# Optimization experiments

Measured on AMD Instinct MI355X. Metric: run time of the kernel, lower is better.

Reference implementation:

```python
import jax, jax.numpy as jnp
import numpy as np

N_NODES = 100000

def _gcn_norm(edge_index, num_nodes):
    # add self-loops, compute symmetric normalization coeffs per edge
    loops = jnp.arange(num_nodes, dtype=edge_index.dtype)
    src = jnp.concatenate([edge_index[0], loops])
    dst = jnp.concatenate([edge_index[1], loops])
    deg = jax.ops.segment_sum(jnp.ones_like(dst, dtype=jnp.float32), dst,
                              num_segments=num_nodes)
    dinv = jnp.where(deg > 0, jax.lax.rsqrt(deg), 0.0)
    norm = dinv[src] * dinv[dst]  # [E + N]
    return src, dst, norm

def _gcn_conv(x, W, b, src, dst, norm, num_nodes):
    h = x @ W                              # [N, out] transform first (PyG order)
    msg = h[src] * norm[:, None]           # gather + scale
    out = jax.ops.segment_sum(msg, dst, num_segments=num_nodes)  # scatter-add
    return out + b

def setup_inputs() -> dict:
    key = jax.random.key(0)
    k1, k2, k3, k4 = jax.random.split(key, 4)
    F_in, H, C = 128, 64, 40
    x = jax.random.normal(k1, (N_NODES, F_in), dtype=jnp.float32)
    edge_index = jax.random.randint(k2, (2, 1600000), 0, N_NODES, dtype=jnp.int64)
    W1 = jax.random.normal(k3, (F_in, H), dtype=jnp.float32) / np.sqrt(F_in)
    b1 = jnp.zeros((H,), dtype=jnp.float32)
    W2 = jax.random.normal(k4, (H, C), dtype=jnp.float32) / np.sqrt(H)
    b2 = jnp.zeros((C,), dtype=jnp.float32)
    return {"x": x, "edge_index": edge_index, "W1": W1, "b1": b1, "W2": W2, "b2": b2}

def reference(x, edge_index, W1, b1, W2, b2):
    num_nodes = x.shape[0]
    src, dst, norm = _gcn_norm(edge_index, num_nodes)
    h = _gcn_conv(x, W1, b1, src, dst, norm, num_nodes)
    h = jax.nn.relu(h)
    # dropout is identity in eval mode (training=False)
    h = _gcn_conv(h, W2, b2, src, dst, norm, num_nodes)
    return jax.nn.log_softmax(h, axis=1)
```

## Files before the change

### kernel.cpp

```cpp
#include <hip/hip_runtime.h>
#include <math.h>

#define NPB 256
#define BSH 8
#define MAXNB 400
#define BIN_CHUNK 8192
#define HIST_CHUNK 16384

typedef __attribute__((ext_vector_type(8))) short bf16x8;
typedef __attribute__((ext_vector_type(4))) float f32x4;
typedef __attribute__((ext_vector_type(2))) float f32x2;

__device__ __forceinline__ unsigned short f2bf(float f){
  unsigned int u = __float_as_uint(f);
  unsigned int r = (u + 0x7FFFu + ((u >> 16) & 1u)) >> 16;
  return (unsigned short)r;
}

__device__ __forceinline__ bf16x8 cvt8(float4 a, float4 b){
  union { unsigned u[4]; bf16x8 v; } r;
  asm("v_cvt_pk_bf16_f32 %0, %1, %2" : "=v"(r.u[0]) : "v"(a.x), "v"(a.y));
  asm("v_cvt_pk_bf16_f32 %0, %1, %2" : "=v"(r.u[1]) : "v"(a.z), "v"(a.w));
  asm("v_cvt_pk_bf16_f32 %0, %1, %2" : "=v"(r.u[2]) : "v"(b.x), "v"(b.y));
  asm("v_cvt_pk_bf16_f32 %0, %1, %2" : "=v"(r.u[3]) : "v"(b.z), "v"(b.w));
  return r.v;
}

__global__ void k_prep(const float* __restrict__ W1, const float* __restrict__ W2,
                       unsigned short* __restrict__ w1t, unsigned short* __restrict__ w2t,
                       int* __restrict__ bcnt, int NB){
  int t = threadIdx.x;
  if(blockIdx.x == 0){
    for(int i = t; i < 8192; i += 256){
      int k = i >> 6, f = i & 63;
      w1t[f*128 + k] = f2bf(W1[i]);
    }
  } else {
    for(int i = t; i < 3072; i += 256){
      int c = i >> 6, k = i & 63;
      w2t[c*64 + k] = (c < 40) ? f2bf(W2[k*40 + c]) : (unsigned short)0;
    }
    for(int i = t; i < NB; i += 256) bcnt[i] = 0;
  }
}


__global__ __launch_bounds__(256) void k_bhist(const int* __restrict__ dst, int E,
                                               int* __restrict__ bcnt, int NB){
  __shared__ int l[MAXNB];
  int t = threadIdx.x;
  int base = blockIdx.x*HIST_CHUNK;
  int end = base + HIST_CHUNK; if(end > E) end = E;
  for(int b = t; b < NB; b += 256) l[b] = 0;
  __syncthreads();
  for(int i = base + t; i < end; i += 256) atomicAdd(&l[dst[i] >> BSH], 1);
  __syncthreads();
  for(int b = t; b < NB; b += 256){ int c = l[b]; if(c) atomicAdd(&bcnt[b], c); }
}

__global__ void k_bscan(const int* __restrict__ bcnt, int* __restrict__ bofs,
                        int* __restrict__ bcur, int NB, int E){
  __shared__ int sh[1024];
  int t = threadIdx.x;
  int c0 = (2*t   < NB) ? bcnt[2*t]   : 0;
  int c1 = (2*t+1 < NB) ? bcnt[2*t+1] : 0;
  sh[t] = c0 + c1; __syncthreads();
  for(int off = 1; off < 1024; off <<= 1){
    int v = (t >= off) ? sh[t - off] : 0;
    __syncthreads();
    sh[t] += v;
    __syncthreads();
  }
  int pairEx = sh[t] - (c0 + c1);
  if(2*t   < NB){ bofs[2*t]   = pairEx;      bcur[2*t]   = pairEx; }
  if(2*t+1 < NB){ bofs[2*t+1] = pairEx + c0; bcur[2*t+1] = pairEx + c0; }
  if(t == 0) bofs[NB] = E;
}

__global__ __launch_bounds__(256) void k_binpass(const int* __restrict__ src,
                          const int* __restrict__ dst, int E,
                          int* __restrict__ bcur, unsigned int* __restrict__ binned, int NB){
  __shared__ int lcnt[MAXNB];
  __shared__ int lpos[MAXNB];
  int t = threadIdx.x;
  int base = blockIdx.x * BIN_CHUNK;
  int end = base + BIN_CHUNK; if(end > E) end = E;
  for(int b = t; b < NB; b += 256) lcnt[b] = 0;
  __syncthreads();
  for(int i = base + t; i < end; i += 256)
    atomicAdd(&lcnt[dst[i] >> BSH], 1);
  __syncthreads();
  for(int b = t; b < NB; b += 256){
    int c = lcnt[b];
    lpos[b] = c ? atomicAdd(&bcur[b], c) : 0;
  }
  __syncthreads();
  for(int i = base + t; i < end; i += 256){
    int d = dst[i];
    int b = d >> BSH;
    unsigned int rec = (unsigned int)src[i] | ((unsigned int)(d & (NPB-1)) << 17);
    int p = atomicAdd(&lpos[b], 1);
    binned[p] = rec;
  }
}

__global__ __launch_bounds__(256) void k_bscatter(const unsigned int* __restrict__ binned,
     const int* __restrict__ bofs, int* __restrict__ csr, int* __restrict__ row_ofs,
     float* __restrict__ dinv, int N, int E, int NB){
  __shared__ int lcnt[NPB];
  __shared__ int lofs[NPB];
  __shared__ int lcur[NPB];
  __shared__ int wsum[4];
  int b = blockIdx.x, t = threadIdx.x;
  int beg = bofs[b], end = bofs[b+1];
  lcnt[t] = 0;
  __syncthreads();
  for(int i = beg + t; i < end; i += 256) atomicAdd(&lcnt[binned[i] >> 17], 1);
  __syncthreads();
  int c = lcnt[t];
  int lane = t & 63, wid = t >> 6;
  int v = c;
  #pragma unroll
  for(int off = 1; off < 64; off <<= 1){
    int nv = __shfl_up(v, off, 64);
    if(lane >= off) v += nv;
  }
  if(lane == 63) wsum[wid] = v;
  __syncthreads();
  int wpre = 0;
  #pragma unroll
  for(int k2 = 0; k2 < 4; k2++) if(k2 < wid) wpre += wsum[k2];
  int ex = wpre + v - c;
  lofs[t] = beg + ex; lcur[t] = 0;
  int node = (b << BSH) + t;
  if(node < N){
    row_ofs[node] = beg + ex;
    dinv[node] = rsqrtf((float)(c + 1));
  }
  __syncthreads();
  for(int i = beg + t; i < end; i += 256){
    unsigned int rec = binned[i];
    int dl = rec >> 17;
    int pos = lofs[dl] + atomicAdd(&lcur[dl], 1);
    csr[pos] = (int)(rec & 0x1FFFFu);
  }
  if(b == NB-1 && t == 0) row_ofs[N] = E;
}

__global__ __launch_bounds__(256) void k_gemm1(const float* __restrict__ x,
                        const unsigned short* __restrict__ w1t,
                        const float* __restrict__ dinv, unsigned int* __restrict__ g1, int n){
  __shared__ unsigned short xs[128*136];
  __shared__ unsigned short wt[64*136];
  int tid = threadIdx.x;
  int nodeBase = blockIdx.x*128;
  for(int i = tid; i < 1024; i += 256){
    int f = i >> 4, seg = i & 15;
    *(uint4*)&wt[f*136 + seg*8] = *(const uint4*)&w1t[f*128 + seg*8];
  }
  {
    const float4* x4 = (const float4*)x;
    for(int i = tid; i < 2048; i += 256){
      int node = i >> 4, seg = i & 15;
      float4 va = make_float4(0.f,0.f,0.f,0.f), vb = va;
      if(nodeBase + node < n){
        va = x4[(size_t)(nodeBase + node)*32 + seg*2];
        vb = x4[(size_t)(nodeBase + node)*32 + seg*2 + 1];
      }
      *(bf16x8*)&xs[node*136 + seg*8] = cvt8(va, vb);
    }
  }
  __syncthreads();

  int w = tid >> 6, lane = tid & 63;
  int ml = lane & 15, q = lane >> 4;
  int n0 = nodeBase + w*32 + ml;
  int n1 = n0 + 16;
  bool vn0 = n0 < n, vn1 = n1 < n;

  f32x4 a00 = {0.f,0.f,0.f,0.f}, a01 = {0.f,0.f,0.f,0.f},
        a02 = {0.f,0.f,0.f,0.f}, a03 = {0.f,0.f,0.f,0.f};
  f32x4 a10 = {0.f,0.f,0.f,0.f}, a11 = {0.f,0.f,0.f,0.f},
        a12 = {0.f,0.f,0.f,0.f}, a13 = {0.f,0.f,0.f,0.f};
  const unsigned short* brow = &xs[(w*32 + ml)*136 + q*8];
  const unsigned short* arow = &wt[ml*136 + q*8];
  #pragma unroll
  for(int s = 0; s < 4; s++){
    bf16x8 bb0 = *(const bf16x8*)(brow +        s*32);
    bf16x8 bb1 = *(const bf16x8*)(brow + 2176 + s*32);
    bf16x8 a0 = *(const bf16x8*)(arow +    0 + s*32);
    bf16x8 a1 = *(const bf16x8*)(arow + 2176 + s*32);
    bf16x8 a2 = *(const bf16x8*)(arow + 4352 + s*32);
    bf16x8 a3 = *(const bf16x8*)(arow + 6528 + s*32);
    a00 = __builtin_amdgcn_mfma_f32_16x16x32_bf16(a0, bb0, a00, 0, 0, 0);
    a01 = __builtin_amdgcn_mfma_f32_16x16x32_bf16(a1, bb0, a01, 0, 0, 0);
    a02 = __builtin_amdgcn_mfma_f32_16x16x32_bf16(a2, bb0, a02, 0, 0, 0);
    a03 = __builtin_amdgcn_mfma_f32_16x16x32_bf16(a3, bb0, a03, 0, 0, 0);
    a10 = __builtin_amdgcn_mfma_f32_16x16x32_bf16(a0, bb1, a10, 0, 0, 0);
    a11 = __builtin_amdgcn_mfma_f32_16x16x32_bf16(a1, bb1, a11, 0, 0, 0);
    a12 = __builtin_amdgcn_mfma_f32_16x16x32_bf16(a2, bb1, a12, 0, 0, 0);
    a13 = __builtin_amdgcn_mfma_f32_16x16x32_bf16(a3, bb1, a13, 0, 0, 0);
  }
  if(vn0){
    float dv = dinv[n0];
    unsigned base16 = ((unsigned)n0 << 4) + q;
    int p;
    p = __builtin_amdgcn_cvt_pk_fp8_f32(a00[0]*dv, a00[1]*dv, 0, false);
    p = __builtin_amdgcn_cvt_pk_fp8_f32(a00[2]*dv, a00[3]*dv, p, true);
    g1[base16 +  0] = (unsigned)p;
    p = __builtin_amdgcn_cvt_pk_fp8_f32(a01[0]*dv, a01[1]*dv, 0, false);
    p = __builtin_amdgcn_cvt_pk_fp8_f32(a01[2]*dv, a01[3]*dv, p, true);
    g1[base16 +  4] = (unsigned)p;
    p = __builtin_amdgcn_cvt_pk_fp8_f32(a02[0]*dv, a02[1]*dv, 0, false);
    p = __builtin_amdgcn_cvt_pk_fp8_f32(a02[2]*dv, a02[3]*dv, p, true);
    g1[base16 +  8] = (unsigned)p;
    p = __builtin_amdgcn_cvt_pk_fp8_f32(a03[0]*dv, a03[1]*dv, 0, false);
    p = __builtin_amdgcn_cvt_pk_fp8_f32(a03[2]*dv, a03[3]*dv, p, true);
    g1[base16 + 12] = (unsigned)p;
  }
  if(vn1){
    float dv = dinv[n1];
    unsigned base16 = ((unsigned)n1 << 4) + q;
    int p;
    p = __builtin_amdgcn_cvt_pk_fp8_f32(a10[0]*dv, a10[1]*dv, 0, false);
    p = __builtin_amdgcn_cvt_pk_fp8_f32(a10[2]*dv, a10[3]*dv, p, true);
    g1[base16 +  0] = (unsigned)p;
    p = __builtin_amdgcn_cvt_pk_fp8_f32(a11[0]*dv, a11[1]*dv, 0, false);
    p = __builtin_amdgcn_cvt_pk_fp8_f32(a11[2]*dv, a11[3]*dv, p, true);
    g1[base16 +  4] = (unsigned)p;
    p = __builtin_amdgcn_cvt_pk_fp8_f32(a12[0]*dv, a12[1]*dv, 0, false);
    p = __builtin_amdgcn_cvt_pk_fp8_f32(a12[2]*dv, a12[3]*dv, p, true);
    g1[base16 +  8] = (unsigned)p;
    p = __builtin_amdgcn_cvt_pk_fp8_f32(a13[0]*dv, a13[1]*dv, 0, false);
    p = __builtin_amdgcn_cvt_pk_fp8_f32(a13[2]*dv, a13[3]*dv, p, true);
    g1[base16 + 12] = (unsigned)p;
  }
}

__global__ __launch_bounds__(256) void k_agg1(const unsigned* __restrict__ g1,
    const int* __restrict__ row_ofs, const int* __restrict__ csr,
    const float* __restrict__ dinv, const float* __restrict__ b1,
    unsigned short* __restrict__ u, int N){
  int t = threadIdx.x;
  int lane = t & 63;
  int f = lane & 15;
  int bq = (lane & 48) << 2;
  int node = blockIdx.x*16 + (t >> 4);
  if(node >= N) return;
  int beg = row_ofs[node], end = row_ofs[node+1];
  unsigned v = g1[((unsigned)node << 4) + f];
  f32x2 s01 = __builtin_amdgcn_cvt_pk_f32_fp8(v, false);
  f32x2 s23 = __builtin_amdgcn_cvt_pk_f32_fp8(v, true);
  for(int e = beg; e < end; e += 16){
    int rem = end - e; if(rem > 16) rem = 16;
    int idxv = (f < rem) ? csr[e + f] : 0;
    int j = 0;
    for(; j + 4 <= rem; j += 4){
      int r0 = __builtin_amdgcn_ds_bpermute(bq + ((j+0) << 2), idxv);
      int r1 = __builtin_amdgcn_ds_bpermute(bq + ((j+1) << 2), idxv);
      int r2 = __builtin_amdgcn_ds_bpermute(bq + ((j+2) << 2), idxv);
      int r3 = __builtin_amdgcn_ds_bpermute(bq + ((j+3) << 2), idxv);
      unsigned v0 = g1[((unsigned)r0 << 4) + f];
      unsigned v1 = g1[((unsigned)r1 << 4) + f];
      unsigned v2 = g1[((unsigned)r2 << 4) + f];
      unsigned v3 = g1[((unsigned)r3 << 4) + f];
      s01 += __builtin_amdgcn_cvt_pk_f32_fp8(v0, false);
      s23 += __builtin_amdgcn_cvt_pk_f32_fp8(v0, true);
      s01 += __builtin_amdgcn_cvt_pk_f32_fp8(v1, false);
      s23 += __builtin_amdgcn_cvt_pk_f32_fp8(v1, true);
      s01 += __builtin_amdgcn_cvt_pk_f32_fp8(v2, false);
      s23 += __builtin_amdgcn_cvt_pk_f32_fp8(v2, true);
      s01 += __builtin_amdgcn_cvt_pk_f32_fp8(v3, false);
      s23 += __builtin_amdgcn_cvt_pk_f32_fp8(v3, true);
    }
    for(; j < rem; j++){
      int r0 = __builtin_amdgcn_ds_bpermute(bq + (j << 2), idxv);
      unsigned v0 = g1[((unsigned)r0 << 4) + f];
      s01 += __builtin_amdgcn_cvt_pk_f32_fp8(v0, false);
      s23 += __builtin_amdgcn_cvt_pk_f32_fp8(v0, true);
    }
  }
  float dv = dinv[node];
  float4 bb = ((const float4*)b1)[f];
  float h0 = fmaxf(fmaf(dv, s01.x, bb.x), 0.f);
  float h1 = fmaxf(fmaf(dv, s01.y, bb.y), 0.f);
  float h2 = fmaxf(fmaf(dv, s23.x, bb.z), 0.f);
  float h3 = fmaxf(fmaf(dv, s23.y, bb.w), 0.f);
  unsigned p0 = (unsigned)f2bf(dv*h0) | ((unsigned)f2bf(dv*h1) << 16);
  unsigned p1 = (unsigned)f2bf(dv*h2) | ((unsigned)f2bf(dv*h3) << 16);
  ((uint2*)u)[((unsigned)node << 4) + f] = make_uint2(p0, p1);
}

__global__ __launch_bounds__(256) void k_gemm2(const unsigned short* __restrict__ u,
                        const unsigned short* __restrict__ w2t,
                        unsigned char* __restrict__ g2, int n){
  __shared__ unsigned short us[64*72];
  __shared__ unsigned short ws2[48*72];
  int t = threadIdx.x;
  int nodeBase = blockIdx.x*64;
  for(int i = t; i < 512; i += 256){
    int row = i >> 3, seg = i & 7;
    uint4 v = make_uint4(0,0,0,0);
    if(nodeBase + row < n) v = *(const uint4*)&u[(size_t)(nodeBase + row)*64 + seg*8];
    *(uint4*)&us[row*72 + seg*8] = v;
  }
  for(int i = t; i < 384; i += 256){
    int row = i >> 3, seg = i & 7;
    *(uint4*)&ws2[row*72 + seg*8] = *(const uint4*)&w2t[row*64 + seg*8];
  }
  __syncthreads();
  int w = t >> 6, lane = t & 63;
  int ml = lane & 15, q = lane >> 4;
  f32x4 acc0 = {0.f,0.f,0.f,0.f}, acc1 = {0.f,0.f,0.f,0.f}, acc2 = {0.f,0.f,0.f,0.f};
  const unsigned short* brow = &us[(w*16 + ml)*72 + q*8];
  const unsigned short* a0r = &ws2[ml*72 + q*8];
  #pragma unroll
  for(int s = 0; s < 2; s++){
    bf16x8 bb = *(const bf16x8*)(brow + s*32);
    bf16x8 a0 = *(const bf16x8*)(a0r +    0 + s*32);
    bf16x8 a1 = *(const bf16x8*)(a0r + 1152 + s*32);
    bf16x8 a2 = *(const bf16x8*)(a0r + 2304 + s*32);
    acc0 = __builtin_amdgcn_mfma_f32_16x16x32_bf16(a0, bb, acc0, 0, 0, 0);
    acc1 = __builtin_amdgcn_mfma_f32_16x16x32_bf16(a1, bb, acc1, 0, 0, 0);
    acc2 = __builtin_amdgcn_mfma_f32_16x16x32_bf16(a2, bb, acc2, 0, 0, 0);
  }
  int node = nodeBase + w*16 + ml;
  if(node < n){
    unsigned* gd = (unsigned*)g2;
    unsigned rb = (unsigned)node*10u + q;
    int p;
    p = __builtin_amdgcn_cvt_pk_fp8_f32(acc0[0], acc0[1], 0, false);
    p = __builtin_amdgcn_cvt_pk_fp8_f32(acc0[2], acc0[3], p, true);
    gd[rb + 0] = (unsigned)p;
    p = __builtin_amdgcn_cvt_pk_fp8_f32(acc1[0], acc1[1], 0, false);
    p = __builtin_amdgcn_cvt_pk_fp8_f32(acc1[2], acc1[3], p, true);
    gd[rb + 4] = (unsigned)p;
    if(q < 2){
      p = __builtin_amdgcn_cvt_pk_fp8_f32(acc2[0], acc2[1], 0, false);
      p = __builtin_amdgcn_cvt_pk_fp8_f32(acc2[2], acc2[3], p, true);
      gd[rb + 8] = (unsigned)p;
    }
  }
}

__global__ __launch_bounds__(256) void k_agg2(const unsigned char* __restrict__ g2,
     const int* __restrict__ row_ofs, const int* __restrict__ csr,
     const float* __restrict__ dinv, const float* __restrict__ b2,
     float* __restrict__ out, int N){
  int t = threadIdx.x;
  int lane = t & 63;
  int f = lane & 15;
  int fc = (f < 10) ? f : 0;
  int bq = (lane & 48) << 2;
  int node = blockIdx.x*16 + (t >> 4);
  if(node >= N) return;
  int beg = row_ofs[node], end = row_ofs[node+1];
  const unsigned* gd = (const unsigned*)g2;
  unsigned v = gd[(unsigned)node*10u + fc];
  f32x2 s01 = __builtin_amdgcn_cvt_pk_f32_fp8(v, false);
  f32x2 s23 = __builtin_amdgcn_cvt_pk_f32_fp8(v, true);
  for(int e = beg; e < end; e += 16){
    int rem = end - e; if(rem > 16) rem = 16;
    int idxv = (f < rem) ? csr[e + f] : 0;
    int j = 0;
    for(; j + 4 <= rem; j += 4){
      int r0 = __builtin_amdgcn_ds_bpermute(bq + ((j+0) << 2), idxv);
      int r1 = __builtin_amdgcn_ds_bpermute(bq + ((j+1) << 2), idxv);
      int r2 = __builtin_amdgcn_ds_bpermute(bq + ((j+2) << 2), idxv);
      int r3 = __builtin_amdgcn_ds_bpermute(bq + ((j+3) << 2), idxv);
      unsigned v0 = gd[(unsigned)r0*10u + fc];
      unsigned v1 = gd[(unsigned)r1*10u + fc];
      unsigned v2 = gd[(unsigned)r2*10u + fc];
      unsigned v3 = gd[(unsigned)r3*10u + fc];
      s01 += __builtin_amdgcn_cvt_pk_f32_fp8(v0, false);
      s23 += __builtin_amdgcn_cvt_pk_f32_fp8(v0, true);
      s01 += __builtin_amdgcn_cvt_pk_f32_fp8(v1, false);
      s23 += __builtin_amdgcn_cvt_pk_f32_fp8(v1, true);
      s01 += __builtin_amdgcn_cvt_pk_f32_fp8(v2, false);
      s23 += __builtin_amdgcn_cvt_pk_f32_fp8(v2, true);
      s01 += __builtin_amdgcn_cvt_pk_f32_fp8(v3, false);
      s23 += __builtin_amdgcn_cvt_pk_f32_fp8(v3, true);
    }
    for(; j < rem; j++){
      int r0 = __builtin_amdgcn_ds_bpermute(bq + (j << 2), idxv);
      unsigned v0 = gd[(unsigned)r0*10u + fc];
      s01 += __builtin_amdgcn_cvt_pk_f32_fp8(v0, false);
      s23 += __builtin_amdgcn_cvt_pk_f32_fp8(v0, true);
    }
  }
  float dv = dinv[node];
  float4 bb = ((const float4*)b2)[fc];
  float l0 = fmaf(dv, s01.x, bb.x);
  float l1 = fmaf(dv, s01.y, bb.y);
  float l2 = fmaf(dv, s23.x, bb.z);
  float l3 = fmaf(dv, s23.y, bb.w);
  bool valid = (f < 10);
  float m = valid ? fmaxf(fmaxf(l0,l1), fmaxf(l2,l3)) : -INFINITY;
  m = fmaxf(m, __shfl_xor(m,1,64)); m = fmaxf(m, __shfl_xor(m,2,64));
  m = fmaxf(m, __shfl_xor(m,4,64)); m = fmaxf(m, __shfl_xor(m,8,64));
  float ex = valid ? (expf(l0-m)+expf(l1-m)) + (expf(l2-m)+expf(l3-m)) : 0.f;
  ex += __shfl_xor(ex,1,64); ex += __shfl_xor(ex,2,64);
  ex += __shfl_xor(ex,4,64); ex += __shfl_xor(ex,8,64);
  float ll = logf(ex);
  if(valid){
    ((float4*)out)[(unsigned)node*10u + f] = make_float4(l0-m-ll, l1-m-ll, l2-m-ll, l3-m-ll);
  }
}


extern "C" void kernel_launch(void* const* d_in, const int* in_sizes, int n_in,
                              void* d_out, int out_size, void* d_ws, size_t ws_size,
                              hipStream_t stream){
  const float* x  = (const float*)d_in[0];
  const int*   ei = (const int*)  d_in[1];
  const float* W1 = (const float*)d_in[2];
  const float* b1 = (const float*)d_in[3];
  const float* W2 = (const float*)d_in[4];
  const float* b2 = (const float*)d_in[5];
  float* out = (float*)d_out;

  int N = in_sizes[0] / 128;
  int E = in_sizes[1] / 2;
  const int* src = ei;
  const int* dst = ei + E;
  int NB = (N + NPB - 1) >> BSH;

  char* w = (char*)d_ws;
  auto alloc = [&](size_t bytes) -> char* {
    char* p = w;
    w += (bytes + 511) & ~(size_t)511;
    return p;
  };
  int*   bcnt    = (int*)  alloc((size_t)NB*4);
  int*   bofs    = (int*)  alloc((size_t)(NB+1)*4);
  int*   bcur    = (int*)  alloc((size_t)NB*4);
  int*   row_ofs = (int*)  alloc((size_t)(N+1)*4);
  float* dinv    = (float*)alloc((size_t)N*4);
  unsigned int* binned = (unsigned int*)alloc((size_t)E*4);
  int*   csr     = (int*)  alloc((size_t)E*4);
  unsigned int*   g1 = (unsigned int*)  alloc((size_t)N*64);
  unsigned short* u  = (unsigned short*)alloc((size_t)N*64*2);
  unsigned char*  g2 = (unsigned char*) alloc((size_t)N*40);
  unsigned short* w1t = (unsigned short*)alloc((size_t)64*128*2);
  unsigned short* w2t = (unsigned short*)alloc((size_t)48*64*2);

  k_prep    <<<2, 256, 0, stream>>>(W1, W2, w1t, w2t, bcnt, NB);
  k_bhist   <<<(E+HIST_CHUNK-1)/HIST_CHUNK, 256, 0, stream>>>(dst, E, bcnt, NB);
  k_bscan   <<<1, 1024, 0, stream>>>(bcnt, bofs, bcur, NB, E);
  k_binpass <<<(E+BIN_CHUNK-1)/BIN_CHUNK, 256, 0, stream>>>(src, dst, E, bcur, binned, NB);
  k_bscatter<<<NB, 256, 0, stream>>>(binned, bofs, csr, row_ofs, dinv, N, E, NB);

  k_gemm1   <<<(N+127)/128, 256, 0, stream>>>(x, w1t, dinv, g1, N);
  k_agg1    <<<(N+15)/16, 256, 0, stream>>>(g1, row_ofs, csr, dinv, b1, u, N);
  k_gemm2   <<<(N+63)/64, 256, 0, stream>>>(u, w2t, g2, N);
  k_agg2    <<<(N+15)/16, 256, 0, stream>>>(g2, row_ofs, csr, dinv, b2, out, N);
}
```

Baseline: 232.3 us.

## Replace binned CSR build with global-atomic counting sort; fuse agg1 into gemm2

The two-level bin-then-scatter CSR construction is replaced by per-node global atomic degree counting, a three-kernel scan, and a direct atomic scatter of source indices into CSR. This drops the intermediate binned buffer and its extra pass, at the cost of global atomics on random destinations. Separately, the layer-1 aggregation is fused into the layer-2 GEMM kernel, which writes aggregated rows into shared memory. That removes the round trip of the intermediate u tensor through global memory but cuts aggregation parallelism to 64 nodes per block.

```diff
diff --git a/kernel.cpp b/kernel.cpp
--- a/kernel.cpp
+++ b/kernel.cpp
@@ -1,11 +1,7 @@
 #include <hip/hip_runtime.h>
 #include <math.h>
 
-#define NPB 256
-#define BSH 8
-#define MAXNB 400
-#define BIN_CHUNK 8192
-#define HIST_CHUNK 16384
+#define HIST_CHUNK 8192
 
 typedef __attribute__((ext_vector_type(8))) short bf16x8;
 typedef __attribute__((ext_vector_type(4))) float f32x4;
@@ -28,42 +24,52 @@
 
 __global__ void k_prep(const float* __restrict__ W1, const float* __restrict__ W2,
                        unsigned short* __restrict__ w1t, unsigned short* __restrict__ w2t,
-                       int* __restrict__ bcnt, int NB){
-  int t = threadIdx.x;
-  if(blockIdx.x == 0){
+                       int* __restrict__ deg, int NPAD){
+  int t = threadIdx.x, b = blockIdx.x;
+  if(b == 0){
     for(int i = t; i < 8192; i += 256){
       int k = i >> 6, f = i & 63;
       w1t[f*128 + k] = f2bf(W1[i]);
     }
-  } else {
+  } else if(b == 1){
     for(int i = t; i < 3072; i += 256){
       int c = i >> 6, k = i & 63;
       w2t[c*64 + k] = (c < 40) ? f2bf(W2[k*40 + c]) : (unsigned short)0;
     }
-    for(int i = t; i < NB; i += 256) bcnt[i] = 0;
-  }
-}
-
-
-__global__ __launch_bounds__(256) void k_bhist(const int* __restrict__ dst, int E,
-                                               int* __restrict__ bcnt, int NB){
-  __shared__ int l[MAXNB];
-  int t = threadIdx.x;
+  } else {
+    int i = (b-2)*256 + t;
+    if(i < NPAD) deg[i] = 0;
+  }
+}
+
+
+__global__ __launch_bounds__(256) void k_hist(const int* __restrict__ dst, int E,
+                                              int* __restrict__ deg){
   int base = blockIdx.x*HIST_CHUNK;
   int end = base + HIST_CHUNK; if(end > E) end = E;
-  for(int b = t; b < NB; b += 256) l[b] = 0;
+  for(int i = base + threadIdx.x; i < end; i += 256)
+    atomicAdd(&deg[dst[i]], 1);
+}
+
+__global__ __launch_bounds__(256) void k_s1(const int* __restrict__ deg,
+                                            int* __restrict__ bsum){
+  __shared__ int ws[4];
+  int b = blockIdx.x, t = threadIdx.x;
+  int v = deg[b*256 + t];
+  v += __shfl_down(v, 32, 64); v += __shfl_down(v, 16, 64);
+  v += __shfl_down(v,  8, 64); v += __shfl_down(v,  4, 64);
+  v += __shfl_down(v,  2, 64); v += __shfl_down(v,  1, 64);
+  if((t & 63) == 0) ws[t >> 6] = v;
   __syncthreads();
-  for(int i = base + t; i < end; i += 256) atomicAdd(&l[dst[i] >> BSH], 1);
-  __syncthreads();
-  for(int b = t; b < NB; b += 256){ int c = l[b]; if(c) atomicAdd(&bcnt[b], c); }
-}
-
-__global__ void k_bscan(const int* __restrict__ bcnt, int* __restrict__ bofs,
-                        int* __restrict__ bcur, int NB, int E){
+  if(t == 0) bsum[b] = ws[0] + ws[1] + ws[2] + ws[3];
+}
+
+__global__ void k_s2(const int* __restrict__ bsum, int* __restrict__ bofs,
+                     int NBK, int E){
   __shared__ int sh[1024];
   int t = threadIdx.x;
-  int c0 = (2*t   < NB) ? bcnt[2*t]   : 0;
-  int c1 = (2*t+1 < NB) ? bcnt[2*t+1] : 0;
+  int c0 = (2*t   < NBK) ? bsum[2*t]   : 0;
+  int c1 = (2*t+1 < NBK) ? bsum[2*t+1] : 0;
   sh[t] = c0 + c1; __syncthreads();
   for(int off = 1; off < 1024; off <<= 1){
     int v = (t >= off) ? sh[t - off] : 0;
@@ -72,52 +78,17 @@
     __syncthreads();
   }
   int pairEx = sh[t] - (c0 + c1);
-  if(2*t   < NB){ bofs[2*t]   = pairEx;      bcur[2*t]   = pairEx; }
-  if(2*t+1 < NB){ bofs[2*t+1] = pairEx + c0; bcur[2*t+1] = pairEx + c0; }
-  if(t == 0) bofs[NB] = E;
-}
-
-__global__ __launch_bounds__(256) void k_binpass(const int* __restrict__ src,
-                          const int* __restrict__ dst, int E,
-                          int* __restrict__ bcur, unsigned int* __restrict__ binned, int NB){
-  __shared__ int lcnt[MAXNB];
-  __shared__ int lpos[MAXNB];
-  int t = threadIdx.x;
-  int base = blockIdx.x * BIN_CHUNK;
-  int end = base + BIN_CHUNK; if(end > E) end = E;
-  for(int b = t; b < NB; b += 256) lcnt[b] = 0;
-  __syncthreads();
-  for(int i = base + t; i < end; i += 256)
-    atomicAdd(&lcnt[dst[i] >> BSH], 1);
-  __syncthreads();
-  for(int b = t; b < NB; b += 256){
-    int c = lcnt[b];
-    lpos[b] = c ? atomicAdd(&bcur[b], c) : 0;
-  }
-  __syncthreads();
-  for(int i = base + t; i < end; i += 256){
-    int d = dst[i];
-    int b = d >> BSH;
-    unsigned int rec = (unsigned int)src[i] | ((unsigned int)(d & (NPB-1)) << 17);
-    int p = atomicAdd(&lpos[b], 1);
-    binned[p] = rec;
-  }
-}
-
-__global__ __launch_bounds__(256) void k_bscatter(const unsigned int* __restrict__ binned,
-     const int* __restrict__ bofs, int* __restrict__ csr, int* __restrict__ row_ofs,
-     float* __restrict__ dinv, int N, int E, int NB){
-  __shared__ int lcnt[NPB];
-  __shared__ int lofs[NPB];
-  __shared__ int lcur[NPB];
+  if(2*t   < NBK) bofs[2*t]   = pairEx;
+  if(2*t+1 < NBK) bofs[2*t+1] = pairEx + c0;
+  if(t == 0) bofs[NBK] = E;
+}
+
+__global__ __launch_bounds__(256) void k_s3(const int* __restrict__ deg,
+     const int* __restrict__ bofs, int* __restrict__ row_ofs, int* __restrict__ cur,
+     float* __restrict__ dinv, int N, int E, int NBK){
   __shared__ int wsum[4];
   int b = blockIdx.x, t = threadIdx.x;
-  int beg = bofs[b], end = bofs[b+1];
-  lcnt[t] = 0;
-  __syncthreads();
-  for(int i = beg + t; i < end; i += 256) atomicAdd(&lcnt[binned[i] >> 17], 1);
-  __syncthreads();
-  int c = lcnt[t];
+  int c = deg[b*256 + t];
   int lane = t & 63, wid = t >> 6;
   int v = c;
   #pragma unroll
@@ -131,20 +102,25 @@
   #pragma unroll
   for(int k2 = 0; k2 < 4; k2++) if(k2 < wid) wpre += wsum[k2];
   int ex = wpre + v - c;
-  lofs[t] = beg + ex; lcur[t] = 0;
-  int node = (b << BSH) + t;
+  int node = b*256 + t;
   if(node < N){
-    row_ofs[node] = beg + ex;
+    int ro = bofs[b] + ex;
+    row_ofs[node] = ro;
+    cur[node] = ro;
     dinv[node] = rsqrtf((float)(c + 1));
   }
-  __syncthreads();
-  for(int i = beg + t; i < end; i += 256){
-    unsigned int rec = binned[i];
-    int dl = rec >> 17;
-    int pos = lofs[dl] + atomicAdd(&lcur[dl], 1);
-    csr[pos] = (int)(rec & 0x1FFFFu);
-  }
-  if(b == NB-1 && t == 0) row_ofs[N] = E;
+  if(b == NBK-1 && t == 0) row_ofs[N] = E;
+}
+
+__global__ __launch_bounds__(256) void k_scatter(const int* __restrict__ src,
+     const int* __restrict__ dst, int E, int* __restrict__ cur, int* __restrict__ csr){
+  int base = blockIdx.x*HIST_CHUNK;
+  int end = base + HIST_CHUNK; if(end > E) end = E;
+  for(int i = base + threadIdx.x; i < end; i += 256){
+    int d = dst[i];
+    int pos = atomicAdd(&cur[d], 1);
+    csr[pos] = src[i];
+  }
 }
 
 __global__ __launch_bounds__(256) void k_gemm1(const float* __restrict__ x,
@@ -237,79 +213,76 @@
   }
 }
 
-__global__ __launch_bounds__(256) void k_agg1(const unsigned* __restrict__ g1,
+__global__ __launch_bounds__(256) void k_agg1g2(const unsigned* __restrict__ g1,
     const int* __restrict__ row_ofs, const int* __restrict__ csr,
     const float* __restrict__ dinv, const float* __restrict__ b1,
-    unsigned short* __restrict__ u, int N){
-  int t = threadIdx.x;
-  int lane = t & 63;
-  int f = lane & 15;
-  int bq = (lane & 48) << 2;
-  int node = blockIdx.x*16 + (t >> 4);
-  if(node >= N) return;
-  int beg = row_ofs[node], end = row_ofs[node+1];
-  unsigned v = g1[((unsigned)node << 4) + f];
-  f32x2 s01 = __builtin_amdgcn_cvt_pk_f32_fp8(v, false);
-  f32x2 s23 = __builtin_amdgcn_cvt_pk_f32_fp8(v, true);
-  for(int e = beg; e < end; e += 16){
-    int rem = end - e; if(rem > 16) rem = 16;
-    int idxv = (f < rem) ? csr[e + f] : 0;
-    int j = 0;
-    for(; j + 4 <= rem; j += 4){
-      int r0 = __builtin_amdgcn_ds_bpermute(bq + ((j+0) << 2), idxv);
-      int r1 = __builtin_amdgcn_ds_bpermute(bq + ((j+1) << 2), idxv);
-      int r2 = __builtin_amdgcn_ds_bpermute(bq + ((j+2) << 2), idxv);
-      int r3 = __builtin_amdgcn_ds_bpermute(bq + ((j+3) << 2), idxv);
-      unsigned v0 = g1[((unsigned)r0 << 4) + f];
-      unsigned v1 = g1[((unsigned)r1 << 4) + f];
-      unsigned v2 = g1[((unsigned)r2 << 4) + f];
-      unsigned v3 = g1[((unsigned)r3 << 4) + f];
-      s01 += __builtin_amdgcn_cvt_pk_f32_fp8(v0, false);
-      s23 += __builtin_amdgcn_cvt_pk_f32_fp8(v0, true);
-      s01 += __builtin_amdgcn_cvt_pk_f32_fp8(v1, false);
-      s23 += __builtin_amdgcn_cvt_pk_f32_fp8(v1, true);
-      s01 += __builtin_amdgcn_cvt_pk_f32_fp8(v2, false);
-      s23 += __builtin_amdgcn_cvt_pk_f32_fp8(v2, true);
-      s01 += __builtin_amdgcn_cvt_pk_f32_fp8(v3, false);
-      s23 += __builtin_amdgcn_cvt_pk_f32_fp8(v3, true);
-    }
-    for(; j < rem; j++){
-      int r0 = __builtin_amdgcn_ds_bpermute(bq + (j << 2), idxv);
-      unsigned v0 = g1[((unsigned)r0 << 4) + f];
-      s01 += __builtin_amdgcn_cvt_pk_f32_fp8(v0, false);
-      s23 += __builtin_amdgcn_cvt_pk_f32_fp8(v0, true);
-    }
-  }
-  float dv = dinv[node];
-  float4 bb = ((const float4*)b1)[f];
-  float h0 = fmaxf(fmaf(dv, s01.x, bb.x), 0.f);
-  float h1 = fmaxf(fmaf(dv, s01.y, bb.y), 0.f);
-  float h2 = fmaxf(fmaf(dv, s23.x, bb.z), 0.f);
-  float h3 = fmaxf(fmaf(dv, s23.y, bb.w), 0.f);
-  unsigned p0 = (unsigned)f2bf(dv*h0) | ((unsigned)f2bf(dv*h1) << 16);
-  unsigned p1 = (unsigned)f2bf(dv*h2) | ((unsigned)f2bf(dv*h3) << 16);
-  ((uint2*)u)[((unsigned)node << 4) + f] = make_uint2(p0, p1);
-}
-
-__global__ __launch_bounds__(256) void k_gemm2(const unsigned short* __restrict__ u,
-                        const unsigned short* __restrict__ w2t,
-                        unsigned char* __restrict__ g2, int n){
+    const unsigned short* __restrict__ w2t, unsigned char* __restrict__ g2, int n){
   __shared__ unsigned short us[64*72];
   __shared__ unsigned short ws2[48*72];
   int t = threadIdx.x;
   int nodeBase = blockIdx.x*64;
-  for(int i = t; i < 512; i += 256){
-    int row = i >> 3, seg = i & 7;
-    uint4 v = make_uint4(0,0,0,0);
-    if(nodeBase + row < n) v = *(const uint4*)&u[(size_t)(nodeBase + row)*64 + seg*8];
-    *(uint4*)&us[row*72 + seg*8] = v;
-  }
   for(int i = t; i < 384; i += 256){
     int row = i >> 3, seg = i & 7;
     *(uint4*)&ws2[row*72 + seg*8] = *(const uint4*)&w2t[row*64 + seg*8];
   }
+  int lane = t & 63;
+  int f = lane & 15;
+  int bq = (lane & 48) << 2;
+  int qg = t >> 4;
+  float4 bb1 = ((const float4*)b1)[f];
+  #pragma unroll 1
+  for(int i = 0; i < 4; i++){
+    int node = nodeBase + qg*4 + i;
+    int lrow = qg*4 + i;
+    if(node < n){
+      int beg = row_ofs[node], end = row_ofs[node+1];
+      unsigned v = g1[((unsigned)node << 4) + f];
+      f32x2 s01 = __builtin_amdgcn_cvt_pk_f32_fp8(v, false);
+      f32x2 s23 = __builtin_amdgcn_cvt_pk_f32_fp8(v, true);
+      for(int e = beg; e < end; e += 16){
+        int rem = end - e; if(rem > 16) rem = 16;
+        int idxv = (f < rem) ? csr[e + f] : 0;
+        int j = 0;
+        for(; j + 4 <= rem; j += 4){
+          int r0 = __builtin_amdgcn_ds_bpermute(bq + ((j+0) << 2), idxv);
+          int r1 = __builtin_amdgcn_ds_bpermute(bq + ((j+1) << 2), idxv);
+          int r2 = __builtin_amdgcn_ds_bpermute(bq + ((j+2) << 2), idxv);
+          int r3 = __builtin_amdgcn_ds_bpermute(bq + ((j+3) << 2), idxv);
+          unsigned v0 = g1[((unsigned)r0 << 4) + f];
+          unsigned v1 = g1[((unsigned)r1 << 4) + f];
+          unsigned v2 = g1[((unsigned)r2 << 4) + f];
+          unsigned v3 = g1[((unsigned)r3 << 4) + f];
+          s01 += __builtin_amdgcn_cvt_pk_f32_fp8(v0, false);
+          s23 += __builtin_amdgcn_cvt_pk_f32_fp8(v0, true);
+          s01 += __builtin_amdgcn_cvt_pk_f32_fp8(v1, false);
+          s23 += __builtin_amdgcn_cvt_pk_f32_fp8(v1, true);
+          s01 += __builtin_amdgcn_cvt_pk_f32_fp8(v2, false);
+          s23 += __builtin_amdgcn_cvt_pk_f32_fp8(v2, true);
+          s01 += __builtin_amdgcn_cvt_pk_f32_fp8(v3, false);
+          s23 += __builtin_amdgcn_cvt_pk_f32_fp8(v3, true);
+        }
+        for(; j < rem; j++){
+          int r0 = __builtin_amdgcn_ds_bpermute(bq + (j << 2), idxv);
+          unsigned v0 = g1[((unsigned)r0 << 4) + f];
+          s01 += __builtin_amdgcn_cvt_pk_f32_fp8(v0, false);
+          s23 += __builtin_amdgcn_cvt_pk_f32_fp8(v0, true);
+        }
+      }
+      float dv = dinv[node];
+      float h0 = fmaxf(fmaf(dv, s01.x, bb1.x), 0.f);
+      float h1 = fmaxf(fmaf(dv, s01.y, bb1.y), 0.f);
+      float h2 = fmaxf(fmaf(dv, s23.x, bb1.z), 0.f);
+      float h3 = fmaxf(fmaf(dv, s23.y, bb1.w), 0.f);
+      unsigned p0, p1;
+      asm("v_cvt_pk_bf16_f32 %0, %1, %2" : "=v"(p0) : "v"(dv*h0), "v"(dv*h1));
+      asm("v_cvt_pk_bf16_f32 %0, %1, %2" : "=v"(p1) : "v"(dv*h2), "v"(dv*h3));
+      *(uint2*)&us[lrow*72 + f*4] = make_uint2(p0, p1);
+    } else {
+      *(uint2*)&us[lrow*72 + f*4] = make_uint2(0u, 0u);
+    }
+  }
   __syncthreads();
-  int w = t >> 6, lane = t & 63;
+  int w = t >> 6;
   int ml = lane & 15, q = lane >> 4;
   f32x4 acc0 = {0.f,0.f,0.f,0.f}, acc1 = {0.f,0.f,0.f,0.f}, acc2 = {0.f,0.f,0.f,0.f};
   const unsigned short* brow = &us[(w*16 + ml)*72 + q*8];
@@ -423,7 +396,8 @@
   int E = in_sizes[1] / 2;
   const int* src = ei;
   const int* dst = ei + E;
-  int NB = (N + NPB - 1) >> BSH;
+  int NBK = (N + 255) >> 8;
+  int NPAD = NBK << 8;
 
   char* w = (char*)d_ws;
   auto alloc = [&](size_t bytes) -> char* {
@@ -431,27 +405,26 @@
     w += (bytes + 511) & ~(size_t)511;
     return p;
   };
-  int*   bcnt    = (int*)  alloc((size_t)NB*4);
-  int*   bofs    = (int*)  alloc((size_t)(NB+1)*4);
-  int*   bcur    = (int*)  alloc((size_t)NB*4);
+  int*   deg     = (int*)  alloc((size_t)NPAD*4);
+  int*   bsum    = (int*)  alloc((size_t)NBK*4);
+  int*   bofs    = (int*)  alloc((size_t)(NBK+1)*4);
   int*   row_ofs = (int*)  alloc((size_t)(N+1)*4);
+  int*   cur     = (int*)  alloc((size_t)N*4);
   float* dinv    = (float*)alloc((size_t)N*4);
-  unsigned int* binned = (unsigned int*)alloc((size_t)E*4);
   int*   csr     = (int*)  alloc((size_t)E*4);
   unsigned int*   g1 = (unsigned int*)  alloc((size_t)N*64);
-  unsigned short* u  = (unsigned short*)alloc((size_t)N*64*2);
   unsigned char*  g2 = (unsigned char*) alloc((size_t)N*40);
   unsigned short* w1t = (unsigned short*)alloc((size_t)64*128*2);
   unsigned short* w2t = (unsigned short*)alloc((size_t)48*64*2);
 
-  k_prep    <<<2, 256, 0, stream>>>(W1, W2, w1t, w2t, bcnt, NB);
-  k_bhist   <<<(E+HIST_CHUNK-1)/HIST_CHUNK, 256, 0, stream>>>(dst, E, bcnt, NB);
-  k_bscan   <<<1, 1024, 0, stream>>>(bcnt, bofs, bcur, NB, E);
-  k_binpass <<<(E+BIN_CHUNK-1)/BIN_CHUNK, 256, 0, stream>>>(src, dst, E, bcur, binned, NB);
-  k_bscatter<<<NB, 256, 0, stream>>>(binned, bofs, csr, row_ofs, dinv, N, E, NB);
+  k_prep    <<<NBK+2, 256, 0, stream>>>(W1, W2, w1t, w2t, deg, NPAD);
+  k_hist    <<<(E+HIST_CHUNK-1)/HIST_CHUNK, 256, 0, stream>>>(dst, E, deg);
+  k_s1      <<<NBK, 256, 0, stream>>>(deg, bsum);
+  k_s2      <<<1, 1024, 0, stream>>>(bsum, bofs, NBK, E);
+  k_s3      <<<NBK, 256, 0, stream>>>(deg, bofs, row_ofs, cur, dinv, N, E, NBK);
+  k_scatter <<<(E+HIST_CHUNK-1)/HIST_CHUNK, 256, 0, stream>>>(src, dst, E, cur, csr);
 
   k_gemm1   <<<(N+127)/128, 256, 0, stream>>>(x, w1t, dinv, g1, N);
-  k_agg1    <<<(N+15)/16, 256, 0, stream>>>(g1, row_ofs, csr, dinv, b1, u, N);
-  k_gemm2   <<<(N+63)/64, 256, 0, stream>>>(u, w2t, g2, N);
+  k_agg1g2  <<<(N+63)/64, 256, 0, stream>>>(g1, row_ofs, csr, dinv, b1, w2t, g2, N);
   k_agg2    <<<(N+15)/16, 256, 0, stream>>>(g2, row_ofs, csr, dinv, b2, out, N);
 }
```

After: 314.3 us. +35.3%, slower.
